# Performance work log

Hardware: AMD Instinct MI355X
Metric: run time of the kernel (lower is better)

The kernel has to match this reference:

```python
import jax, jax.numpy as jnp
import numpy as np

N, E, C, L = 50000, 800000, 64, 3  # nodes, edges, channels, message-passing layers
EPS = 1e-5  # torch.nn.LayerNorm default eps


def _mlp(h, W0, b0, W1, b1, W2, b2, g, beta):
    # MLP(input, hidden=[C, C], output=C) with ReLU between linears, LayerNorm at end
    h = jax.nn.relu(h @ W0 + b0)
    h = jax.nn.relu(h @ W1 + b1)
    h = h @ W2 + b2
    mu = jnp.mean(h, axis=-1, keepdims=True)
    var = jnp.var(h, axis=-1, keepdims=True)
    return (h - mu) * jax.lax.rsqrt(var + EPS) * g + beta


def setup_inputs() -> dict:
    key = jax.random.key(0)
    ks = jax.random.split(key, 12)
    def w(k, shape, fan_in):
        return (jax.random.normal(k, shape, jnp.float32) / np.float32(np.sqrt(fan_in)))
    return {
        "x": jax.random.normal(ks[0], (N, C), jnp.float32),
        "e": jax.random.normal(ks[1], (E, C), jnp.float32),
        "edge_index": jax.random.randint(ks[2], (2, E), 0, N),
        # edge_updater MLP params, stacked over L layers
        "ew0": w(ks[3], (L, 3 * C, C), 3 * C), "eb0": jnp.zeros((L, C), jnp.float32),
        "ew1": w(ks[4], (L, C, C), C),         "eb1": jnp.zeros((L, C), jnp.float32),
        "ew2": w(ks[5], (L, C, C), C),         "eb2": jnp.zeros((L, C), jnp.float32),
        "eg": jnp.ones((L, C), jnp.float32),   "ebt": jnp.zeros((L, C), jnp.float32),
        # node_updater MLP params
        "nw0": w(ks[6], (L, 2 * C, C), 2 * C), "nb0": jnp.zeros((L, C), jnp.float32),
        "nw1": w(ks[7], (L, C, C), C),         "nb1": jnp.zeros((L, C), jnp.float32),
        "nw2": w(ks[8], (L, C, C), C),         "nb2": jnp.zeros((L, C), jnp.float32),
        "ng": jnp.ones((L, C), jnp.float32),   "nbt": jnp.zeros((L, C), jnp.float32),
    }


def reference(x, e, edge_index, ew0, eb0, ew1, eb1, ew2, eb2, eg, ebt,
              nw0, nb0, nw1, nb1, nw2, nb2, ng, nbt):
    src, dst = edge_index[0], edge_index[1]
    for i in range(L):
        # e += edge_updater(cat(x_src, x_dst, e))
        e = e + _mlp(jnp.concatenate([x[src], x[dst], e], axis=1),
                     ew0[i], eb0[i], ew1[i], eb1[i], ew2[i], eb2[i], eg[i], ebt[i])
        # EdgeAggregation(aggr='add'): scatter-add edge features at target nodes
        agg = jax.ops.segment_sum(e, dst, num_segments=N)
        # x += node_updater(cat(x, agg))
        x = x + _mlp(jnp.concatenate([x, agg], axis=1),
                     nw0[i], nb0[i], nw1[i], nb1[i], nw2[i], nb2[i], ng[i], nbt[i])
    return (x, e)
```

## Files before the change

### kernel.cpp

```cpp
#include <hip/hip_runtime.h>

#define CH 64

using bf16x8 = __attribute__((ext_vector_type(8))) short;
using f32x4  = __attribute__((ext_vector_type(4))) float;

__device__ __forceinline__ unsigned short f2bf(float f) {
  unsigned int u = __float_as_uint(f);
  u = (u + 0x7FFFu + ((u >> 16) & 1u)) >> 16;
  return (unsigned short)u;
}

__device__ __forceinline__ bf16x8 pack8(f32x4 a, f32x4 b) {
  bf16x8 r;
  r[0] = (short)f2bf(a[0]); r[1] = (short)f2bf(a[1]);
  r[2] = (short)f2bf(a[2]); r[3] = (short)f2bf(a[3]);
  r[4] = (short)f2bf(b[0]); r[5] = (short)f2bf(b[1]);
  r[6] = (short)f2bf(b[2]); r[7] = (short)f2bf(b[3]);
  return r;
}

#define E0S 200
#define S64 72
#define N0S 136

#define EW0_L 0
#define EW1_L 12800
#define EW2_L 17408
#define EW_TOT 22016
#define E_LDS 31232

#define NW0_L 0
#define NW1_L 8704
#define NW2_L 13312
#define NW_TOT 17920
#define N_LDS 22528

#define WS_NW 66048
#define WS_AGG_B    262144
#define WS_ROWPTR_B 13062144
#define WS_NEXT_B   13262208
#define WS_EID_B    13462208

__global__ void prep_w(const float* __restrict__ ew0, const float* __restrict__ ew1,
                       const float* __restrict__ ew2, const float* __restrict__ nw0,
                       const float* __restrict__ nw1, const float* __restrict__ nw2,
                       unsigned short* __restrict__ ws) {
  int i = blockIdx.x * 256 + threadIdx.x;
  if (i < 36864) {
    int l = i / 12288, r = i % 12288, k = r / 64, n = r % 64;
    ws[l * EW_TOT + EW0_L + n * E0S + k] = f2bf(ew0[i]);
  } else if (i < 49152) {
    int j = i - 36864, l = j / 4096, r = j % 4096, k = r / 64, n = r % 64;
    ws[l * EW_TOT + EW1_L + n * S64 + k] = f2bf(ew1[j]);
  } else if (i < 61440) {
    int j = i - 49152, l = j / 4096, r = j % 4096, k = r / 64, n = r % 64;
    ws[l * EW_TOT + EW2_L + n * S64 + k] = f2bf(ew2[j]);
  } else if (i < 86016) {
    int j = i - 61440, l = j / 8192, r = j % 8192, k = r / 64, n = r % 64;
    ws[WS_NW + l * NW_TOT + NW0_L + n * N0S + k] = f2bf(nw0[j]);
  } else if (i < 98304) {
    int j = i - 86016, l = j / 4096, r = j % 4096, k = r / 64, n = r % 64;
    ws[WS_NW + l * NW_TOT + NW1_L + n * S64 + k] = f2bf(nw1[j]);
  } else if (i < 110592) {
    int j = i - 98304, l = j / 4096, r = j % 4096, k = r / 64, n = r % 64;
    ws[WS_NW + l * NW_TOT + NW2_L + n * S64 + k] = f2bf(nw2[j]);
  }
}

__global__ void hist_k(const int* __restrict__ dst, int* __restrict__ counts, int nE) {
  int i = blockIdx.x * 256 + threadIdx.x;
  if (i < nE) atomicAdd(counts + dst[i], 1);
}

__global__ void scan_k(const int* __restrict__ counts, int* __restrict__ row_ptr,
                       int* __restrict__ next, int n) {
  __shared__ int wsum[16];
  __shared__ int chunk_tot;
  __shared__ int base_sh;
  const int tid = threadIdx.x, lane = tid & 63, wv = tid >> 6;
  if (tid == 0) { base_sh = 0; row_ptr[0] = 0; }
  __syncthreads();
  for (int start = 0; start < n; start += 4096) {
    int idx = start + tid * 4;
    int v[4], s = 0;
#pragma unroll
    for (int k = 0; k < 4; ++k) { v[k] = (idx + k < n) ? counts[idx + k] : 0; s += v[k]; }
    int incl = s;
#pragma unroll
    for (int off = 1; off < 64; off <<= 1) {
      int t = __shfl_up(incl, off, 64);
      if (lane >= off) incl += t;
    }
    if (lane == 63) wsum[wv] = incl;
    __syncthreads();
    if (wv == 0 && lane < 16) {
      int w = wsum[lane];
      int wincl = w;
#pragma unroll
      for (int off = 1; off < 16; off <<= 1) {
        int t = __shfl_up(wincl, off, 16);
        if (lane >= off) wincl += t;
      }
      if (lane == 15) chunk_tot = wincl;
      wsum[lane] = wincl - w;
    }
    __syncthreads();
    int run = base_sh + wsum[wv] + (incl - s);
#pragma unroll
    for (int k = 0; k < 4; ++k) {
      int i = idx + k;
      if (i < n) { next[i] = run; run += v[k]; row_ptr[i + 1] = run; }
    }
    __syncthreads();
    if (tid == 0) base_sh += chunk_tot;
    __syncthreads();
  }
}

__global__ void scatter_k(const int* __restrict__ dst, int* __restrict__ next,
                          int* __restrict__ eid, int nE) {
  int i = blockIdx.x * 256 + threadIdx.x;
  if (i < nE) {
    int p = atomicAdd(next + dst[i], 1);
    eid[p] = i;
  }
}

__global__ __launch_bounds__(512, 4)
void edge_kernel(const float* __restrict__ x, const float* e_in, float* e_out,
                 const int* __restrict__ src, const int* __restrict__ dst,
                 const unsigned short* __restrict__ wg,
                 const float* __restrict__ b0, const float* __restrict__ b1,
                 const float* __restrict__ b2, const float* __restrict__ gam,
                 const float* __restrict__ bet, int nE) {
  __shared__ unsigned short lds[E_LDS];
  const int tid = threadIdx.x;
  {
    const uint4* s4 = (const uint4*)wg;
    uint4* d4 = (uint4*)lds;
    for (int i = tid; i < EW_TOT / 8; i += 512) d4[i] = s4[i];
  }
  __syncthreads();

  const int wave = tid >> 6, lane = tid & 63;
  const int quad = lane >> 4, l15 = lane & 15;
  const int h1o = EW_TOT + wave * 1152;

  float b0c[4], b1c[4], b2c[4], gc[4], btc[4];
#pragma unroll
  for (int j = 0; j < 4; ++j) {
    int col = j * 16 + l15;
    b0c[j] = b0[col]; b1c[j] = b1[col]; b2c[j] = b2[col];
    gc[j] = gam[col]; btc[j] = bet[col];
  }

  const int o1 = quad * 8, o2 = 32 + quad * 8;

  for (int base = blockIdx.x * 128; base < nE; base += gridDim.x * 128) {
    const int ebase = base + wave * 16;
    const int row = ebase + l15;
    int si = src[row], di = dst[row];
    const float* xs = x + (size_t)si * CH;
    const float* xd = x + (size_t)di * CH;
    const float* er = e_in + (size_t)row * CH;
    bf16x8 af[6];
    {
      f32x4 a0 = *(const f32x4*)(xs + o1);
      f32x4 a1 = *(const f32x4*)(xs + o1 + 4);
      f32x4 a2 = *(const f32x4*)(xs + o2);
      f32x4 a3 = *(const f32x4*)(xs + o2 + 4);
      af[0] = pack8(a0, a1); af[1] = pack8(a2, a3);
    }
    {
      f32x4 a0 = *(const f32x4*)(xd + o1);
      f32x4 a1 = *(const f32x4*)(xd + o1 + 4);
      f32x4 a2 = *(const f32x4*)(xd + o2);
      f32x4 a3 = *(const f32x4*)(xd + o2 + 4);
      af[2] = pack8(a0, a1); af[3] = pack8(a2, a3);
    }
    {
      f32x4 a0 = *(const f32x4*)(er + o1);
      f32x4 a1 = *(const f32x4*)(er + o1 + 4);
      f32x4 a2 = *(const f32x4*)(er + o2);
      f32x4 a3 = *(const f32x4*)(er + o2 + 4);
      af[4] = pack8(a0, a1); af[5] = pack8(a2, a3);
    }

    f32x4 acc0[4];
#pragma unroll
    for (int j = 0; j < 4; ++j) acc0[j] = (f32x4){0.f, 0.f, 0.f, 0.f};
#pragma unroll
    for (int t = 0; t < 6; ++t) {
#pragma unroll
      for (int j = 0; j < 4; ++j) {
        bf16x8 b = *(const bf16x8*)(lds + EW0_L + (j * 16 + l15) * E0S + t * 32 + quad * 8);
        acc0[j] = __builtin_amdgcn_mfma_f32_16x16x32_bf16(af[t], b, acc0[j], 0, 0, 0);
      }
    }
#pragma unroll
    for (int j = 0; j < 4; ++j) {
      int col = j * 16 + l15;
#pragma unroll
      for (int r = 0; r < 4; ++r) {
        float v = fmaxf(acc0[j][r] + b0c[j], 0.f);
        lds[h1o + (quad * 4 + r) * S64 + col] = f2bf(v);
      }
    }
    f32x4 acc1[4];
#pragma unroll
    for (int j = 0; j < 4; ++j) acc1[j] = (f32x4){0.f, 0.f, 0.f, 0.f};
#pragma unroll
    for (int t = 0; t < 2; ++t) {
      bf16x8 a = *(const bf16x8*)(lds + h1o + l15 * S64 + t * 32 + quad * 8);
#pragma unroll
      for (int j = 0; j < 4; ++j) {
        bf16x8 b = *(const bf16x8*)(lds + EW1_L + (j * 16 + l15) * S64 + t * 32 + quad * 8);
        acc1[j] = __builtin_amdgcn_mfma_f32_16x16x32_bf16(a, b, acc1[j], 0, 0, 0);
      }
    }
#pragma unroll
    for (int j = 0; j < 4; ++j) {
      int col = j * 16 + l15;
#pragma unroll
      for (int r = 0; r < 4; ++r) {
        float v = fmaxf(acc1[j][r] + b1c[j], 0.f);
        lds[h1o + (quad * 4 + r) * S64 + col] = f2bf(v);
      }
    }
    f32x4 acc2[4];
#pragma unroll
    for (int j = 0; j < 4; ++j) acc2[j] = (f32x4){0.f, 0.f, 0.f, 0.f};
#pragma unroll
    for (int t = 0; t < 2; ++t) {
      bf16x8 a = *(const bf16x8*)(lds + h1o + l15 * S64 + t * 32 + quad * 8);
#pragma unroll
      for (int j = 0; j < 4; ++j) {
        bf16x8 b = *(const bf16x8*)(lds + EW2_L + (j * 16 + l15) * S64 + t * 32 + quad * 8);
        acc2[j] = __builtin_amdgcn_mfma_f32_16x16x32_bf16(a, b, acc2[j], 0, 0, 0);
      }
    }
    float vv[4][4], s1[4], s2[4];
#pragma unroll
    for (int r = 0; r < 4; ++r) { s1[r] = 0.f; s2[r] = 0.f; }
#pragma unroll
    for (int j = 0; j < 4; ++j)
#pragma unroll
      for (int r = 0; r < 4; ++r) {
        float v = acc2[j][r] + b2c[j];
        vv[j][r] = v; s1[r] += v; s2[r] += v * v;
      }
#pragma unroll
    for (int m = 1; m < 16; m <<= 1)
#pragma unroll
      for (int r = 0; r < 4; ++r) {
        s1[r] += __shfl_xor(s1[r], m, 64);
        s2[r] += __shfl_xor(s2[r], m, 64);
      }
#pragma unroll
    for (int r = 0; r < 4; ++r) {
      int eidx = ebase + quad * 4 + r;
      float mean = s1[r] * 0.015625f;
      float var = s2[r] * 0.015625f - mean * mean;
      float rstd = rsqrtf(var + 1e-5f);
      const float* ein_row = e_in + (size_t)eidx * CH;
      float* eout_row = e_out + (size_t)eidx * CH;
#pragma unroll
      for (int j = 0; j < 4; ++j) {
        int col = j * 16 + l15;
        float y = (vv[j][r] - mean) * rstd * gc[j] + btc[j];
        eout_row[col] = ein_row[col] + y;
      }
    }
  }
}

__global__ __launch_bounds__(256)
void agg_kernel(const float* __restrict__ e, const int* __restrict__ row_ptr,
                const int* __restrict__ eid, float* __restrict__ agg, int nN) {
  int node = blockIdx.x * 4 + (threadIdx.x >> 6);
  if (node >= nN) return;
  int lane = threadIdx.x & 63;
  int quad = lane >> 4, l15 = lane & 15;
  int r0 = row_ptr[node], r1 = row_ptr[node + 1];
  f32x4 s = (f32x4){0.f, 0.f, 0.f, 0.f};
  f32x4 s2 = (f32x4){0.f, 0.f, 0.f, 0.f};
  int i = r0 + quad;
  for (; i + 4 < r1; i += 8) {
    int e0 = eid[i], e1 = eid[i + 4];
    f32x4 a = *(const f32x4*)(e + (size_t)e0 * CH + l15 * 4);
    f32x4 b = *(const f32x4*)(e + (size_t)e1 * CH + l15 * 4);
    s += a; s2 += b;
  }
  for (; i < r1; i += 4) {
    int e0 = eid[i];
    s += *(const f32x4*)(e + (size_t)e0 * CH + l15 * 4);
  }
  s += s2;
#pragma unroll
  for (int c = 0; c < 4; ++c) {
    s[c] += __shfl_xor(s[c], 16, 64);
    s[c] += __shfl_xor(s[c], 32, 64);
  }
  if (quad == 0) *(f32x4*)(agg + (size_t)node * CH + l15 * 4) = s;
}

__global__ __launch_bounds__(256, 3)
void node_kernel(const float* x_in, const float* __restrict__ agg_in,
                 const unsigned short* __restrict__ wg,
                 const float* __restrict__ b0, const float* __restrict__ b1,
                 const float* __restrict__ b2, const float* __restrict__ gam,
                 const float* __restrict__ bet, float* x_out, int nN) {
  __shared__ unsigned short lds[N_LDS];
  const int tid = threadIdx.x;
  {
    const uint4* s4 = (const uint4*)wg;
    uint4* d4 = (uint4*)lds;
    for (int i = tid; i < NW_TOT / 8; i += 256) d4[i] = s4[i];
  }
  __syncthreads();

  const int wave = tid >> 6, lane = tid & 63;
  const int quad = lane >> 4, l15 = lane & 15;
  const int h1o = NW_TOT + wave * 1152;

  float b0c[4], b1c[4], b2c[4], gc[4], btc[4];
#pragma unroll
  for (int j = 0; j < 4; ++j) {
    int col = j * 16 + l15;
    b0c[j] = b0[col]; b1c[j] = b1[col]; b2c[j] = b2[col];
    gc[j] = gam[col]; btc[j] = bet[col];
  }

  const int o1 = quad * 8, o2 = 32 + quad * 8;

  for (int base = blockIdx.x * 64; base < nN; base += gridDim.x * 64) {
    const int nbase = base + wave * 16;
    if (nbase >= nN) continue;
    const int row = nbase + l15;
    const float* xr = x_in + (size_t)row * CH;
    const float* ar = agg_in + (size_t)row * CH;
    bf16x8 af[4];
    {
      f32x4 a0 = *(const f32x4*)(xr + o1);
      f32x4 a1 = *(const f32x4*)(xr + o1 + 4);
      f32x4 a2 = *(const f32x4*)(xr + o2);
      f32x4 a3 = *(const f32x4*)(xr + o2 + 4);
      af[0] = pack8(a0, a1); af[1] = pack8(a2, a3);
    }
    {
      f32x4 a0 = *(const f32x4*)(ar + o1);
      f32x4 a1 = *(const f32x4*)(ar + o1 + 4);
      f32x4 a2 = *(const f32x4*)(ar + o2);
      f32x4 a3 = *(const f32x4*)(ar + o2 + 4);
      af[2] = pack8(a0, a1); af[3] = pack8(a2, a3);
    }

    f32x4 acc0[4];
#pragma unroll
    for (int j = 0; j < 4; ++j) acc0[j] = (f32x4){0.f, 0.f, 0.f, 0.f};
#pragma unroll
    for (int t = 0; t < 4; ++t) {
#pragma unroll
      for (int j = 0; j < 4; ++j) {
        bf16x8 b = *(const bf16x8*)(lds + NW0_L + (j * 16 + l15) * N0S + t * 32 + quad * 8);
        acc0[j] = __builtin_amdgcn_mfma_f32_16x16x32_bf16(af[t], b, acc0[j], 0, 0, 0);
      }
    }
#pragma unroll
    for (int j = 0; j < 4; ++j) {
      int col = j * 16 + l15;
#pragma unroll
      for (int r = 0; r < 4; ++r) {
        float v = fmaxf(acc0[j][r] + b0c[j], 0.f);
        lds[h1o + (quad * 4 + r) * S64 + col] = f2bf(v);
      }
    }
    f32x4 acc1[4];
#pragma unroll
    for (int j = 0; j < 4; ++j) acc1[j] = (f32x4){0.f, 0.f, 0.f, 0.f};
#pragma unroll
    for (int t = 0; t < 2; ++t) {
      bf16x8 a = *(const bf16x8*)(lds + h1o + l15 * S64 + t * 32 + quad * 8);
#pragma unroll
      for (int j = 0; j < 4; ++j) {
        bf16x8 b = *(const bf16x8*)(lds + NW1_L + (j * 16 + l15) * S64 + t * 32 + quad * 8);
        acc1[j] = __builtin_amdgcn_mfma_f32_16x16x32_bf16(a, b, acc1[j], 0, 0, 0);
      }
    }
#pragma unroll
    for (int j = 0; j < 4; ++j) {
      int col = j * 16 + l15;
#pragma unroll
      for (int r = 0; r < 4; ++r) {
        float v = fmaxf(acc1[j][r] + b1c[j], 0.f);
        lds[h1o + (quad * 4 + r) * S64 + col] = f2bf(v);
      }
    }
    f32x4 acc2[4];
#pragma unroll
    for (int j = 0; j < 4; ++j) acc2[j] = (f32x4){0.f, 0.f, 0.f, 0.f};
#pragma unroll
    for (int t = 0; t < 2; ++t) {
      bf16x8 a = *(const bf16x8*)(lds + h1o + l15 * S64 + t * 32 + quad * 8);
#pragma unroll
      for (int j = 0; j < 4; ++j) {
        bf16x8 b = *(const bf16x8*)(lds + NW2_L + (j * 16 + l15) * S64 + t * 32 + quad * 8);
        acc2[j] = __builtin_amdgcn_mfma_f32_16x16x32_bf16(a, b, acc2[j], 0, 0, 0);
      }
    }
    float vv[4][4], s1[4], s2[4];
#pragma unroll
    for (int r = 0; r < 4; ++r) { s1[r] = 0.f; s2[r] = 0.f; }
#pragma unroll
    for (int j = 0; j < 4; ++j)
#pragma unroll
      for (int r = 0; r < 4; ++r) {
        float v = acc2[j][r] + b2c[j];
        vv[j][r] = v; s1[r] += v; s2[r] += v * v;
      }
#pragma unroll
    for (int m = 1; m < 16; m <<= 1)
#pragma unroll
      for (int r = 0; r < 4; ++r) {
        s1[r] += __shfl_xor(s1[r], m, 64);
        s2[r] += __shfl_xor(s2[r], m, 64);
      }
#pragma unroll
    for (int r = 0; r < 4; ++r) {
      int node = nbase + quad * 4 + r;
      float mean = s1[r] * 0.015625f;
      float var = s2[r] * 0.015625f - mean * mean;
      float rstd = rsqrtf(var + 1e-5f);
      const float* xin_row = x_in + (size_t)node * CH;
      float* xout_row = x_out + (size_t)node * CH;
#pragma unroll
      for (int j = 0; j < 4; ++j) {
        int col = j * 16 + l15;
        float y = (vv[j][r] - mean) * rstd * gc[j] + btc[j];
        xout_row[col] = xin_row[col] + y;
      }
    }
  }
}

extern "C" void kernel_launch(void* const* d_in, const int* in_sizes, int n_in,
                              void* d_out, int out_size, void* d_ws, size_t ws_size,
                              hipStream_t stream) {
  const float* x0 = (const float*)d_in[0];
  const float* e0 = (const float*)d_in[1];
  const int* ei  = (const int*)d_in[2];
  const float* ew0 = (const float*)d_in[3];
  const float* eb0 = (const float*)d_in[4];
  const float* ew1 = (const float*)d_in[5];
  const float* eb1 = (const float*)d_in[6];
  const float* ew2 = (const float*)d_in[7];
  const float* eb2 = (const float*)d_in[8];
  const float* eg  = (const float*)d_in[9];
  const float* ebt = (const float*)d_in[10];
  const float* nw0 = (const float*)d_in[11];
  const float* nb0 = (const float*)d_in[12];
  const float* nw1 = (const float*)d_in[13];
  const float* nb1 = (const float*)d_in[14];
  const float* nw2 = (const float*)d_in[15];
  const float* nb2 = (const float*)d_in[16];
  const float* ng  = (const float*)d_in[17];
  const float* nbt = (const float*)d_in[18];

  const int N = in_sizes[0] / CH;
  const int E = in_sizes[1] / CH;
  const int* src = ei;
  const int* dst = ei + E;

  float* xout = (float*)d_out;
  float* eout = (float*)d_out + (size_t)N * CH;

  unsigned short* wsu = (unsigned short*)d_ws;
  float* agg    = (float*)((char*)d_ws + WS_AGG_B);
  int* row_ptr  = (int*)((char*)d_ws + WS_ROWPTR_B);
  int* nxt      = (int*)((char*)d_ws + WS_NEXT_B);
  int* eid      = (int*)((char*)d_ws + WS_EID_B);

  prep_w<<<432, 256, 0, stream>>>(ew0, ew1, ew2, nw0, nw1, nw2, wsu);

  hipMemsetAsync(nxt, 0, (size_t)N * sizeof(int), stream);
  hist_k<<<(E + 255) / 256, 256, 0, stream>>>(dst, nxt, E);
  scan_k<<<1, 1024, 0, stream>>>(nxt, row_ptr, nxt, N);
  scatter_k<<<(E + 255) / 256, 256, 0, stream>>>(dst, nxt, eid, E);

  for (int l = 0; l < 3; ++l) {
    const float* xin = (l == 0) ? x0 : xout;
    const float* einp = (l == 0) ? e0 : eout;
    edge_kernel<<<512, 512, 0, stream>>>(
        xin, einp, eout, src, dst, wsu + l * EW_TOT,
        eb0 + l * CH, eb1 + l * CH, eb2 + l * CH, eg + l * CH, ebt + l * CH, E);
    agg_kernel<<<(N + 3) / 4, 256, 0, stream>>>(eout, row_ptr, eid, agg, N);
    node_kernel<<<768, 256, 0, stream>>>(
        xin, agg, wsu + WS_NW + l * NW_TOT,
        nb0 + l * CH, nb1 + l * CH, nb2 + l * CH, ng + l * CH, nbt + l * CH,
        xout, N);
  }
}
```

Before: 1.056 ms.

## Vectorize residual epilogue via LDS transpose and prefetch next edge indices

The LayerNorm output is staged through a per-wave LDS buffer so each lane can write its row with 16-byte vector stores. The residual input row is reused from registers loaded at the start instead of being re-read from global memory. The edge kernel also loads the next iteration's src/dst indices early to hide gather latency, and the node kernel grid grows to 782 blocks. This costs more LDS per block, which may lower occupancy, plus extra LDS traffic and register pressure.

```diff
diff --git a/kernel.cpp b/kernel.cpp
--- a/kernel.cpp
+++ b/kernel.cpp
@@ -23,18 +23,19 @@
 #define E0S 200
 #define S64 72
 #define N0S 136
+#define Y68 68
 
 #define EW0_L 0
 #define EW1_L 12800
 #define EW2_L 17408
 #define EW_TOT 22016
-#define E_LDS 31232
+#define E_LDS 39424
 
 #define NW0_L 0
 #define NW1_L 8704
 #define NW2_L 13312
 #define NW_TOT 17920
-#define N_LDS 22528
+#define N_LDS 26624
 
 #define WS_NW 66048
 #define WS_AGG_B    262144
@@ -145,7 +146,8 @@
 
   const int wave = tid >> 6, lane = tid & 63;
   const int quad = lane >> 4, l15 = lane & 15;
-  const int h1o = EW_TOT + wave * 1152;
+  const int EHo = EW_TOT + wave * 2176;
+  float* yb = (float*)(lds + EHo);
 
   float b0c[4], b1c[4], b2c[4], gc[4], btc[4];
 #pragma unroll
@@ -156,14 +158,20 @@
   }
 
   const int o1 = quad * 8, o2 = 32 + quad * 8;
-
-  for (int base = blockIdx.x * 128; base < nE; base += gridDim.x * 128) {
-    const int ebase = base + wave * 16;
-    const int row = ebase + l15;
-    int si = src[row], di = dst[row];
+  const int gstride = gridDim.x * 128;
+
+  int row0 = blockIdx.x * 128 + wave * 16 + l15;
+  int si = src[row0], di = dst[row0];
+
+  for (int base = blockIdx.x * 128; base < nE; base += gstride) {
+    const int row = base + wave * 16 + l15;
+    const float* er = e_in + (size_t)row * CH;
+    f32x4 ve0 = *(const f32x4*)(er + o1);
+    f32x4 ve1 = *(const f32x4*)(er + o1 + 4);
+    f32x4 ve2 = *(const f32x4*)(er + o2);
+    f32x4 ve3 = *(const f32x4*)(er + o2 + 4);
     const float* xs = x + (size_t)si * CH;
     const float* xd = x + (size_t)di * CH;
-    const float* er = e_in + (size_t)row * CH;
     bf16x8 af[6];
     {
       f32x4 a0 = *(const f32x4*)(xs + o1);
@@ -179,12 +187,14 @@
       f32x4 a3 = *(const f32x4*)(xd + o2 + 4);
       af[2] = pack8(a0, a1); af[3] = pack8(a2, a3);
     }
+    af[4] = pack8(ve0, ve1); af[5] = pack8(ve2, ve3);
+
     {
-      f32x4 a0 = *(const f32x4*)(er + o1);
-      f32x4 a1 = *(const f32x4*)(er + o1 + 4);
-      f32x4 a2 = *(const f32x4*)(er + o2);
-      f32x4 a3 = *(const f32x4*)(er + o2 + 4);
-      af[4] = pack8(a0, a1); af[5] = pack8(a2, a3);
+      int nbase = base + gstride;
+      if (nbase < nE) {
+        int nrow = nbase + wave * 16 + l15;
+        si = src[nrow]; di = dst[nrow];
+      }
     }
 
     f32x4 acc0[4];
@@ -204,7 +214,7 @@
 #pragma unroll
       for (int r = 0; r < 4; ++r) {
         float v = fmaxf(acc0[j][r] + b0c[j], 0.f);
-        lds[h1o + (quad * 4 + r) * S64 + col] = f2bf(v);
+        lds[EHo + (quad * 4 + r) * S64 + col] = f2bf(v);
       }
     }
     f32x4 acc1[4];
@@ -212,7 +222,7 @@
     for (int j = 0; j < 4; ++j) acc1[j] = (f32x4){0.f, 0.f, 0.f, 0.f};
 #pragma unroll
     for (int t = 0; t < 2; ++t) {
-      bf16x8 a = *(const bf16x8*)(lds + h1o + l15 * S64 + t * 32 + quad * 8);
+      bf16x8 a = *(const bf16x8*)(lds + EHo + l15 * S64 + t * 32 + quad * 8);
 #pragma unroll
       for (int j = 0; j < 4; ++j) {
         bf16x8 b = *(const bf16x8*)(lds + EW1_L + (j * 16 + l15) * S64 + t * 32 + quad * 8);
@@ -225,7 +235,7 @@
 #pragma unroll
       for (int r = 0; r < 4; ++r) {
         float v = fmaxf(acc1[j][r] + b1c[j], 0.f);
-        lds[h1o + (quad * 4 + r) * S64 + col] = f2bf(v);
+        lds[EHo + (quad * 4 + r) * S64 + col] = f2bf(v);
       }
     }
     f32x4 acc2[4];
@@ -233,7 +243,7 @@
     for (int j = 0; j < 4; ++j) acc2[j] = (f32x4){0.f, 0.f, 0.f, 0.f};
 #pragma unroll
     for (int t = 0; t < 2; ++t) {
-      bf16x8 a = *(const bf16x8*)(lds + h1o + l15 * S64 + t * 32 + quad * 8);
+      bf16x8 a = *(const bf16x8*)(lds + EHo + l15 * S64 + t * 32 + quad * 8);
 #pragma unroll
       for (int j = 0; j < 4; ++j) {
         bf16x8 b = *(const bf16x8*)(lds + EW2_L + (j * 16 + l15) * S64 + t * 32 + quad * 8);
@@ -259,19 +269,24 @@
       }
 #pragma unroll
     for (int r = 0; r < 4; ++r) {
-      int eidx = ebase + quad * 4 + r;
       float mean = s1[r] * 0.015625f;
       float var = s2[r] * 0.015625f - mean * mean;
       float rstd = rsqrtf(var + 1e-5f);
-      const float* ein_row = e_in + (size_t)eidx * CH;
-      float* eout_row = e_out + (size_t)eidx * CH;
-#pragma unroll
-      for (int j = 0; j < 4; ++j) {
-        int col = j * 16 + l15;
+#pragma unroll
+      for (int j = 0; j < 4; ++j) {
         float y = (vv[j][r] - mean) * rstd * gc[j] + btc[j];
-        eout_row[col] = ein_row[col] + y;
-      }
-    }
+        yb[(quad * 4 + r) * Y68 + j * 16 + l15] = y;
+      }
+    }
+    f32x4 y0 = *(const f32x4*)(yb + l15 * Y68 + o1);
+    f32x4 y1 = *(const f32x4*)(yb + l15 * Y68 + o1 + 4);
+    f32x4 y2 = *(const f32x4*)(yb + l15 * Y68 + o2);
+    f32x4 y3 = *(const f32x4*)(yb + l15 * Y68 + o2 + 4);
+    float* eo = e_out + (size_t)row * CH;
+    *(f32x4*)(eo + o1)     = ve0 + y0;
+    *(f32x4*)(eo + o1 + 4) = ve1 + y1;
+    *(f32x4*)(eo + o2)     = ve2 + y2;
+    *(f32x4*)(eo + o2 + 4) = ve3 + y3;
   }
 }
 
@@ -322,7 +337,8 @@
 
   const int wave = tid >> 6, lane = tid & 63;
   const int quad = lane >> 4, l15 = lane & 15;
-  const int h1o = NW_TOT + wave * 1152;
+  const int NHo = NW_TOT + wave * 2176;
+  float* yb = (float*)(lds + NHo);
 
   float b0c[4], b1c[4], b2c[4], gc[4], btc[4];
 #pragma unroll
@@ -340,14 +356,12 @@
     const int row = nbase + l15;
     const float* xr = x_in + (size_t)row * CH;
     const float* ar = agg_in + (size_t)row * CH;
+    f32x4 vx0 = *(const f32x4*)(xr + o1);
+    f32x4 vx1 = *(const f32x4*)(xr + o1 + 4);
+    f32x4 vx2 = *(const f32x4*)(xr + o2);
+    f32x4 vx3 = *(const f32x4*)(xr + o2 + 4);
     bf16x8 af[4];
-    {
-      f32x4 a0 = *(const f32x4*)(xr + o1);
-      f32x4 a1 = *(const f32x4*)(xr + o1 + 4);
-      f32x4 a2 = *(const f32x4*)(xr + o2);
-      f32x4 a3 = *(const f32x4*)(xr + o2 + 4);
-      af[0] = pack8(a0, a1); af[1] = pack8(a2, a3);
-    }
+    af[0] = pack8(vx0, vx1); af[1] = pack8(vx2, vx3);
     {
       f32x4 a0 = *(const f32x4*)(ar + o1);
       f32x4 a1 = *(const f32x4*)(ar + o1 + 4);
@@ -373,7 +387,7 @@
 #pragma unroll
       for (int r = 0; r < 4; ++r) {
         float v = fmaxf(acc0[j][r] + b0c[j], 0.f);
-        lds[h1o + (quad * 4 + r) * S64 + col] = f2bf(v);
+        lds[NHo + (quad * 4 + r) * S64 + col] = f2bf(v);
       }
     }
     f32x4 acc1[4];
@@ -381,7 +395,7 @@
     for (int j = 0; j < 4; ++j) acc1[j] = (f32x4){0.f, 0.f, 0.f, 0.f};
 #pragma unroll
     for (int t = 0; t < 2; ++t) {
-      bf16x8 a = *(const bf16x8*)(lds + h1o + l15 * S64 + t * 32 + quad * 8);
+      bf16x8 a = *(const bf16x8*)(lds + NHo + l15 * S64 + t * 32 + quad * 8);
 #pragma unroll
       for (int j = 0; j < 4; ++j) {
         bf16x8 b = *(const bf16x8*)(lds + NW1_L + (j * 16 + l15) * S64 + t * 32 + quad * 8);
@@ -394,7 +408,7 @@
 #pragma unroll
       for (int r = 0; r < 4; ++r) {
         float v = fmaxf(acc1[j][r] + b1c[j], 0.f);
-        lds[h1o + (quad * 4 + r) * S64 + col] = f2bf(v);
+        lds[NHo + (quad * 4 + r) * S64 + col] = f2bf(v);
       }
     }
     f32x4 acc2[4];
@@ -402,7 +416,7 @@
     for (int j = 0; j < 4; ++j) acc2[j] = (f32x4){0.f, 0.f, 0.f, 0.f};
 #pragma unroll
     for (int t = 0; t < 2; ++t) {
-      bf16x8 a = *(const bf16x8*)(lds + h1o + l15 * S64 + t * 32 + quad * 8);
+      bf16x8 a = *(const bf16x8*)(lds + NHo + l15 * S64 + t * 32 + quad * 8);
 #pragma unroll
       for (int j = 0; j < 4; ++j) {
         bf16x8 b = *(const bf16x8*)(lds + NW2_L + (j * 16 + l15) * S64 + t * 32 + quad * 8);
@@ -428,19 +442,24 @@
       }
 #pragma unroll
     for (int r = 0; r < 4; ++r) {
-      int node = nbase + quad * 4 + r;
       float mean = s1[r] * 0.015625f;
       float var = s2[r] * 0.015625f - mean * mean;
       float rstd = rsqrtf(var + 1e-5f);
-      const float* xin_row = x_in + (size_t)node * CH;
-      float* xout_row = x_out + (size_t)node * CH;
-#pragma unroll
-      for (int j = 0; j < 4; ++j) {
-        int col = j * 16 + l15;
+#pragma unroll
+      for (int j = 0; j < 4; ++j) {
         float y = (vv[j][r] - mean) * rstd * gc[j] + btc[j];
-        xout_row[col] = xin_row[col] + y;
-      }
-    }
+        yb[(quad * 4 + r) * Y68 + j * 16 + l15] = y;
+      }
+    }
+    f32x4 y0 = *(const f32x4*)(yb + l15 * Y68 + o1);
+    f32x4 y1 = *(const f32x4*)(yb + l15 * Y68 + o1 + 4);
+    f32x4 y2 = *(const f32x4*)(yb + l15 * Y68 + o2);
+    f32x4 y3 = *(const f32x4*)(yb + l15 * Y68 + o2 + 4);
+    float* xo = x_out + (size_t)row * CH;
+    *(f32x4*)(xo + o1)     = vx0 + y0;
+    *(f32x4*)(xo + o1 + 4) = vx1 + y1;
+    *(f32x4*)(xo + o2)     = vx2 + y2;
+    *(f32x4*)(xo + o2 + 4) = vx3 + y3;
   }
 }
 
@@ -495,7 +514,7 @@
         xin, einp, eout, src, dst, wsu + l * EW_TOT,
         eb0 + l * CH, eb1 + l * CH, eb2 + l * CH, eg + l * CH, ebt + l * CH, E);
     agg_kernel<<<(N + 3) / 4, 256, 0, stream>>>(eout, row_ptr, eid, agg, N);
-    node_kernel<<<768, 256, 0, stream>>>(
+    node_kernel<<<782, 256, 0, stream>>>(
         xin, agg, wsu + WS_NW + l * NW_TOT,
         nb0 + l * CH, nb1 + l * CH, nb2 + l * CH, ng + l * CH, nbt + l * CH,
         xout, N);
```

New measurement: 969.9 us. 8.1% less time.
